# Kernel tuning notes

Measured on AMD Instinct MI355X. Metric: run time of the kernel, lower is better.

## Reference

```python
import jax, jax.numpy as jnp
import numpy as np

B, T, C, H = 2, 2048, 1024, 16
HS = C // H  # 64
EPS = 1e-5


def layer_norm(x, w, b):
    mu = jnp.mean(x, axis=-1, keepdims=True)
    var = jnp.var(x, axis=-1, keepdims=True)
    return (x - mu) * jax.lax.rsqrt(var + EPS) * w + b


def setup_inputs() -> dict:
    key = jax.random.key(0)
    ks = jax.random.split(key, 16)
    s_c = 1.0 / np.sqrt(C)
    s_f = 1.0 / np.sqrt(4 * C)
    u = lambda k, shape, s: jax.random.uniform(k, shape, jnp.float32, -s, s)
    return {
        "x": jax.random.normal(ks[0], (B, T, C), jnp.float32),
        # per-head Q/K/V Linears stacked over heads: [H, C, HS], bias [H, HS]
        "Wq": u(ks[1], (H, C, HS), s_c), "bq": u(ks[2], (H, HS), s_c),
        "Wk": u(ks[3], (H, C, HS), s_c), "bk": u(ks[4], (H, HS), s_c),
        "Wv": u(ks[5], (H, C, HS), s_c), "bv": u(ks[6], (H, HS), s_c),
        "Wp": u(ks[7], (C, C), s_c), "bp": u(ks[8], (C,), s_c),
        "W1": u(ks[9], (C, 4 * C), s_c), "b1": u(ks[10], (4 * C,), s_c),
        "W2": u(ks[11], (4 * C, C), s_f), "b2": u(ks[12], (C,), s_f),
        "ln1_w": jnp.ones((C,), jnp.float32), "ln1_b": jnp.zeros((C,), jnp.float32),
        "ln2_w": jnp.ones((C,), jnp.float32), "ln2_b": jnp.zeros((C,), jnp.float32),
    }


def reference(x, Wq, bq, Wk, bk, Wv, bv, Wp, bp, W1, b1, W2, b2,
              ln1_w, ln1_b, ln2_w, ln2_b):
    # --- pre-norm self-attention ---
    xn = layer_norm(x, ln1_w, ln1_b)
    q = jnp.einsum('btc,hcd->bhtd', xn, Wq) + bq[None, :, None, :]
    k = jnp.einsum('btc,hcd->bhtd', xn, Wk) + bk[None, :, None, :]
    v = jnp.einsum('btc,hcd->bhtd', xn, Wv) + bv[None, :, None, :]
    # NOTE: original scales by C**-0.5 (full embedding dim), not head_size**-0.5
    att = jnp.einsum('bhtd,bhsd->bhts', q, k) * (C ** -0.5)
    att = jax.nn.softmax(att, axis=-1)
    o = jnp.einsum('bhts,bhsd->bhtd', att, v)  # [B,H,T,HS]
    o = jnp.transpose(o, (0, 2, 1, 3)).reshape(B, T, C)  # concat heads
    sa = o @ Wp + bp
    out = x + sa
    # --- pre-norm FFN (exact erf GELU, matching nn.GELU default) ---
    on = layer_norm(out, ln2_w, ln2_b)
    h = jax.nn.gelu(on @ W1 + b1, approximate=False)
    return out + (h @ W2 + b2)
```

## Files before the change

kernel.cpp:

```cpp
#include <hip/hip_runtime.h>
#include <math.h>

#define BB 2
#define TT 2048
#define CC 1024
#define HH 16
#define HS 64
#define MT 4096
#define FF 4096

typedef unsigned short u16;
typedef __bf16 bfrag __attribute__((ext_vector_type(8)));
typedef float f4 __attribute__((ext_vector_type(4)));
typedef float f16v __attribute__((ext_vector_type(16)));

#define AS1(p) ((const __attribute__((address_space(1))) void*)(p))
#define AS3(p) ((__attribute__((address_space(3))) void*)(p))

__device__ __forceinline__ u16 f2bf(float f) {
  union { float f; unsigned u; } a; a.f = f;
  return (u16)((a.u + 0x7fffu + ((a.u >> 16) & 1u)) >> 16);
}
__device__ __forceinline__ float bf2f(u16 u) {
  union { unsigned u; float f; } a; a.u = ((unsigned)u) << 16; return a.f;
}

__device__ __forceinline__ int swz128(int byteoff) {
  return byteoff ^ (((byteoff >> 7) & 7) << 4);
}
__device__ __forceinline__ int swzAB(int byteoff) {
  return byteoff ^ (((byteoff >> 7) & 3) << 4);
}

#define XCD_SWZ_2D(BX, BY)                                                     \
  int _fl = (int)blockIdx.y * gridDim.x + blockIdx.x;                          \
  const int _nw = gridDim.x * gridDim.y;                                       \
  _fl = (_fl & 7) * (_nw >> 3) + (_fl >> 3);                                   \
  const int BX = _fl % gridDim.x;                                              \
  const int BY = _fl / gridDim.x;

__global__ void tr_f32_bf16(const float* __restrict__ src, u16* __restrict__ dst,
                            int R, int Cc, long long sb, long long db, int dld) {
  __shared__ float t[32][33];
  const int bz = blockIdx.z;
  const int r0 = blockIdx.y * 32, c0 = blockIdx.x * 32;
  const int tx = threadIdx.x, ty = threadIdx.y;
  const float* s = src + bz * sb;
  u16* d = dst + bz * db;
#pragma unroll
  for (int i = 0; i < 4; i++)
    t[ty + i * 8][tx] = s[(size_t)(r0 + ty + i * 8) * Cc + c0 + tx];
  __syncthreads();
#pragma unroll
  for (int i = 0; i < 4; i++)
    d[(size_t)(c0 + ty + i * 8) * dld + r0 + tx] = f2bf(t[tx][ty + i * 8]);
}

__global__ void tr_bf16(const u16* __restrict__ src, u16* __restrict__ dst,
                        int R, int Cc, long long sb, long long db, int dld) {
  __shared__ u16 t[32][33];
  const int bz = blockIdx.z;
  const int r0 = blockIdx.y * 32, c0 = blockIdx.x * 32;
  const int tx = threadIdx.x, ty = threadIdx.y;
  const u16* s = src + bz * sb;
  u16* d = dst + bz * db;
#pragma unroll
  for (int i = 0; i < 4; i++)
    t[ty + i * 8][tx] = s[(size_t)(r0 + ty + i * 8) * Cc + c0 + tx];
  __syncthreads();
#pragma unroll
  for (int i = 0; i < 4; i++)
    d[(size_t)(c0 + ty + i * 8) * dld + r0 + tx] = t[tx][ty + i * 8];
}

__global__ __launch_bounds__(256) void ln_kernel(
    const float* __restrict__ x, const float* __restrict__ w,
    const float* __restrict__ b, u16* __restrict__ y) {
  const int row = blockIdx.x, tid = threadIdx.x;
  const float4 v = reinterpret_cast<const float4*>(x + (size_t)row * CC)[tid];
  float s = v.x + v.y + v.z + v.w;
  float s2 = v.x * v.x + v.y * v.y + v.z * v.z + v.w * v.w;
#pragma unroll
  for (int off = 32; off >= 1; off >>= 1) {
    s += __shfl_xor(s, off);
    s2 += __shfl_xor(s2, off);
  }
  __shared__ float ps[4], ps2[4];
  const int wave = tid >> 6, lane = tid & 63;
  if (lane == 0) { ps[wave] = s; ps2[wave] = s2; }
  __syncthreads();
  s = ps[0] + ps[1] + ps[2] + ps[3];
  s2 = ps2[0] + ps2[1] + ps2[2] + ps2[3];
  const float mu = s * (1.f / CC);
  const float rstd = rsqrtf(s2 * (1.f / CC) - mu * mu + 1e-5f);
  const float4 wv = reinterpret_cast<const float4*>(w)[tid];
  const float4 bv = reinterpret_cast<const float4*>(b)[tid];
  ushort4 o;
  o.x = f2bf((v.x - mu) * rstd * wv.x + bv.x);
  o.y = f2bf((v.y - mu) * rstd * wv.y + bv.y);
  o.z = f2bf((v.z - mu) * rstd * wv.z + bv.z);
  o.w = f2bf((v.w - mu) * rstd * wv.w + bv.w);
  reinterpret_cast<ushort4*>(y + (size_t)row * CC)[tid] = o;
}

template<int NJ>
__device__ __forceinline__ void gemm_core(
    u16* smem, const u16* __restrict__ A, const u16* __restrict__ Bt,
    int K, int lda, int ldb, int bmi, int bni, f4 (&acc)[4][NJ]) {
  constexpr int BN = NJ * 32;
  constexpr int BBUF = BN * 32;
  u16* As = smem;
  u16* Bs = smem + 3 * 4096;
  const int tid = threadIdx.x;
  const int wave = tid >> 6, lane = tid & 63;
  const int wm = wave >> 1, wn = wave & 1;
  const int lg = lane >> 4, ll = lane & 15;

  const int trow = tid >> 2;
  const int tch  = (tid & 3) ^ ((trow >> 1) & 3);
  const u16* ga = A + (size_t)(bmi * 128 + trow) * lda + tch * 8;
  const u16* gb = Bt + (size_t)(bni * BN + trow) * ldb + tch * 8;
  const size_t g64a = (size_t)64 * lda;
  const size_t g64b = (size_t)64 * ldb;
  const int nt = K >> 5;

  auto GSTAGE = [&](int bi, int kt) {
    u16* la = &As[bi * 4096 + tid * 8];
    u16* lb = &Bs[bi * BBUF + tid * 8];
    const u16* gA = ga + kt * 32;
    const u16* gB = gb + kt * 32;
    __builtin_amdgcn_global_load_lds(AS1(gA), AS3(la), 16, 0, 0);
    __builtin_amdgcn_global_load_lds(AS1(gA + g64a), AS3(la + 2048), 16, 0, 0);
    __builtin_amdgcn_global_load_lds(AS1(gB), AS3(lb), 16, 0, 0);
    if constexpr (NJ == 4)
      __builtin_amdgcn_global_load_lds(AS1(gB + g64b), AS3(lb + 2048), 16, 0, 0);
  };

  GSTAGE(0, 0);
  GSTAGE(1, 1);
  GSTAGE(2, 2);
  int bi = 0;
  for (int t = 0; t < nt; t++) {
    const int ahead = nt - 1 - t;
    if constexpr (NJ == 4) {
      if (ahead >= 2)      asm volatile("s_waitcnt vmcnt(8)" ::: "memory");
      else if (ahead == 1) asm volatile("s_waitcnt vmcnt(4)" ::: "memory");
      else                 asm volatile("s_waitcnt vmcnt(0)" ::: "memory");
    } else {
      if (ahead >= 2)      asm volatile("s_waitcnt vmcnt(6)" ::: "memory");
      else if (ahead == 1) asm volatile("s_waitcnt vmcnt(3)" ::: "memory");
      else                 asm volatile("s_waitcnt vmcnt(0)" ::: "memory");
    }
    __builtin_amdgcn_s_barrier();
    __builtin_amdgcn_sched_barrier(0);

    const char* as_ = (const char*)(As + bi * 4096);
    const char* bs_ = (const char*)(Bs + bi * BBUF);
    bfrag af[4], bf[NJ];
#pragma unroll
    for (int i = 0; i < 4; i++)
      af[i] = *(const bfrag*)(as_ + swzAB((wm * 64 + i * 16 + ll) * 64 + lg * 16));
#pragma unroll
    for (int j = 0; j < NJ; j++)
      bf[j] = *(const bfrag*)(bs_ + swzAB((wn * (BN / 2) + j * 16 + ll) * 64 + lg * 16));

    __builtin_amdgcn_s_setprio(1);
#pragma unroll
    for (int i = 0; i < 4; i++)
#pragma unroll
      for (int j = 0; j < NJ; j++)
        acc[i][j] = __builtin_amdgcn_mfma_f32_16x16x32_bf16(af[i], bf[j], acc[i][j], 0, 0, 0);
    __builtin_amdgcn_s_setprio(0);

    __builtin_amdgcn_sched_barrier(0);
    __builtin_amdgcn_s_barrier();
    if (t + 3 < nt) GSTAGE(bi, t + 3);
    bi = (bi == 2) ? 0 : bi + 1;
  }
}

#define EPI_COORDS                                              \
  const int tid = threadIdx.x;                                  \
  const int wave = tid >> 6, lane = tid & 63;                   \
  const int wm = wave >> 1, wn = wave & 1;                      \
  const int lg = lane >> 4, ll = lane & 15;

__global__ __launch_bounds__(256, 3) void gemm_qkv(
    const u16* __restrict__ A, const u16* __restrict__ Bt,
    const float* __restrict__ bq, const float* __restrict__ bk,
    const float* __restrict__ bv,
    u16* __restrict__ q, u16* __restrict__ k, u16* __restrict__ v) {
  __shared__ u16 smem[24576];
  XCD_SWZ_2D(bx, by)
  f4 acc[4][4] = {};
  gemm_core<4>(smem, A, Bt, CC, CC, CC, by, bx, acc);
  EPI_COORDS
  __syncthreads();
#pragma unroll
  for (int j = 0; j < 4; j++) {
    const int n = bx * 128 + wn * 64 + j * 16 + ll;
    const int sec = n >> 10, nn = n & 1023;
    const float bias = (sec == 0 ? bq : (sec == 1 ? bk : bv))[nn];
    const float scale = (sec == 0) ? 0.045084220027780106f : 1.0f;
#pragma unroll
    for (int i = 0; i < 4; i++)
#pragma unroll
      for (int r = 0; r < 4; r++)
        smem[(wm * 64 + i * 16 + lg * 4 + r) * 136 + wn * 64 + j * 16 + ll] =
            f2bf((acc[i][j][r] + bias) * scale);
  }
  __syncthreads();
  const int rr = tid >> 4, cb = (tid & 15) * 8;
#pragma unroll
  for (int R = 0; R < 8; R++) {
    const int row = R * 16 + rr;
    const int m = by * 128 + row, b = m >> 11, t = m & 2047;
    const int n = bx * 128 + cb;
    const int sec = n >> 10, nn = n & 1023, h = nn >> 6, d = nn & 63;
    u16* dst = sec == 0 ? q : (sec == 1 ? k : v);
    *(uint4*)&dst[(((size_t)b * HH + h) * TT + t) * HS + d] =
        *(const uint4*)&smem[row * 136 + cb];
  }
}

__global__ __launch_bounds__(256, 3) void gemm_ffn1(
    const u16* __restrict__ A, const u16* __restrict__ Bt,
    const float* __restrict__ b1, u16* __restrict__ hb) {
  __shared__ u16 smem[24576];
  XCD_SWZ_2D(bx, by)
  f4 acc[4][4] = {};
  gemm_core<4>(smem, A, Bt, CC, CC, CC, by, bx, acc);
  EPI_COORDS
  __syncthreads();
#pragma unroll
  for (int j = 0; j < 4; j++) {
    const int n = bx * 128 + wn * 64 + j * 16 + ll;
    const float bias = b1[n];
#pragma unroll
    for (int i = 0; i < 4; i++)
#pragma unroll
      for (int r = 0; r < 4; r++) {
        const float t = acc[i][j][r] + bias;
        const float g = 0.5f * t * (1.0f + erff(t * 0.70710678118654752f));
        smem[(wm * 64 + i * 16 + lg * 4 + r) * 136 + wn * 64 + j * 16 + ll] = f2bf(g);
      }
  }
  __syncthreads();
  const int rr = tid >> 4, cb = (tid & 15) * 8;
#pragma unroll
  for (int R = 0; R < 8; R++) {
    const int row = R * 16 + rr;
    *(uint4*)&hb[(size_t)(by * 128 + row) * FF + bx * 128 + cb] =
        *(const uint4*)&smem[row * 136 + cb];
  }
}

__global__ __launch_bounds__(256, 3) void gemm_ffn2sk(
    const u16* __restrict__ A, const u16* __restrict__ Bt,
    u16* __restrict__ p0, u16* __restrict__ p1) {
  __shared__ u16 smem[24576];
  int _fl = ((int)blockIdx.z * gridDim.y + blockIdx.y) * gridDim.x + blockIdx.x;
  const int _nw = gridDim.x * gridDim.y * gridDim.z;
  _fl = (_fl & 7) * (_nw >> 3) + (_fl >> 3);
  const int bx = _fl % gridDim.x;
  const int by = (_fl / gridDim.x) % gridDim.y;
  const int bz = _fl / (gridDim.x * gridDim.y);

  f4 acc[4][4] = {};
  gemm_core<4>(smem, A + bz * 2048, Bt + bz * 2048, 2048, FF, FF, by, bx, acc);
  EPI_COORDS
  __syncthreads();
#pragma unroll
  for (int j = 0; j < 4; j++)
#pragma unroll
    for (int i = 0; i < 4; i++)
#pragma unroll
      for (int r = 0; r < 4; r++)
        smem[(wm * 64 + i * 16 + lg * 4 + r) * 136 + wn * 64 + j * 16 + ll] =
            f2bf(acc[i][j][r]);
  __syncthreads();
  u16* pp = bz ? p1 : p0;
  const int rr = tid >> 4, cb = (tid & 15) * 8;
#pragma unroll
  for (int R = 0; R < 8; R++) {
    const int row = R * 16 + rr;
    *(uint4*)&pp[(size_t)(by * 128 + row) * CC + bx * 128 + cb] =
        *(const uint4*)&smem[row * 136 + cb];
  }
}

__global__ __launch_bounds__(256) void ffn2_reduce(
    const u16* __restrict__ p0, const u16* __restrict__ p1,
    const float* __restrict__ b2, float* __restrict__ dout) {
  const int gid = blockIdx.x * 256 + threadIdx.x;
  const int n0 = (gid * 8) & (CC - 1);
  const uint4 a = ((const uint4*)p0)[gid];
  const uint4 c = ((const uint4*)p1)[gid];
  const u16* au = (const u16*)&a;
  const u16* cu = (const u16*)&c;
  float4 d0 = ((const float4*)dout)[gid * 2];
  float4 d1 = ((const float4*)dout)[gid * 2 + 1];
  const float4 w0 = *(const float4*)&b2[n0];
  const float4 w1 = *(const float4*)&b2[n0 + 4];
  d0.x += w0.x + bf2f(au[0]) + bf2f(cu[0]);
  d0.y += w0.y + bf2f(au[1]) + bf2f(cu[1]);
  d0.z += w0.z + bf2f(au[2]) + bf2f(cu[2]);
  d0.w += w0.w + bf2f(au[3]) + bf2f(cu[3]);
  d1.x += w1.x + bf2f(au[4]) + bf2f(cu[4]);
  d1.y += w1.y + bf2f(au[5]) + bf2f(cu[5]);
  d1.z += w1.z + bf2f(au[6]) + bf2f(cu[6]);
  d1.w += w1.w + bf2f(au[7]) + bf2f(cu[7]);
  ((float4*)dout)[gid * 2] = d0;
  ((float4*)dout)[gid * 2 + 1] = d1;
}

__global__ __launch_bounds__(256, 3) void gemm_proj(
    const u16* __restrict__ A, const u16* __restrict__ Bt,
    const float* __restrict__ bp, const float* __restrict__ x,
    float* __restrict__ outw) {
  __shared__ u16 smem[18432];
  XCD_SWZ_2D(bx, by)
  f4 acc[4][2] = {};
  gemm_core<2>(smem, A, Bt, CC, CC, CC, by, bx, acc);
  EPI_COORDS
#pragma unroll
  for (int i = 0; i < 4; i++)
#pragma unroll
    for (int j = 0; j < 2; j++) {
      const int n = bx * 64 + wn * 32 + j * 16 + ll;
      const float bias = bp[n];
#pragma unroll
      for (int r = 0; r < 4; r++) {
        const int m = by * 128 + wm * 64 + i * 16 + lg * 4 + r;
        const size_t idx = (size_t)m * CC + n;
        outw[idx] = acc[i][j][r] + bias + x[idx];
      }
    }
}

__global__ __launch_bounds__(256, 2) void attn_kernel(
    const u16* __restrict__ Q, const u16* __restrict__ Kb,
    const u16* __restrict__ Vt, u16* __restrict__ Ao) {
  __shared__ __align__(1024) u16 Ks[2][64 * 64];
  __shared__ __align__(1024) u16 Vs[2][64 * 64];

  const int fl = (int)blockIdx.y * gridDim.x + blockIdx.x;
  const int idx = fl >> 3;
  const int bh = (idx >> 4) * 8 + (fl & 7);
  const int qt = idx & 15;

  const int tid = threadIdx.x, wave = tid >> 6, lane = tid & 63;
  const int l31 = lane & 31, hi = lane >> 5;

  bfrag qf[4];
  const u16* Qb = Q + ((size_t)bh * TT + qt * 128 + wave * 32) * HS;
#pragma unroll
  for (int t = 0; t < 4; t++)
    qf[t] = *(const bfrag*)&Qb[l31 * HS + t * 16 + hi * 8];

  f16v o0 = {}, o1 = {};
  float mrun = -INFINITY, lrun = 0.f;

  const int trow = tid >> 3;
  const int tch  = (tid & 7) ^ (trow & 7);
  const u16* gk = Kb + ((size_t)bh * TT + trow) * HS + tch * 8;
  const u16* gv = Vt + ((size_t)bh * HS + trow) * TT + tch * 8;

  int koff[2][4], voff[2][2][2];
#pragma unroll
  for (int sub = 0; sub < 2; sub++) {
#pragma unroll
    for (int t = 0; t < 4; t++)
      koff[sub][t] = swz128((sub * 32 + l31) * 128 + t * 32 + hi * 16);
#pragma unroll
    for (int dh = 0; dh < 2; dh++)
#pragma unroll
      for (int ks = 0; ks < 2; ks++)
        voff[dh][sub][ks] = swz128((dh * 32 + l31) * 128 + sub * 64 + ks * 32 + hi * 16);
  }

#define STAGE(bufi, stt)                                                          \
  do {                                                                            \
    u16* lk = &Ks[bufi][tid * 8];                                                 \
    u16* lv = &Vs[bufi][tid * 8];                                                 \
    __builtin_amdgcn_global_load_lds(AS1(gk + (size_t)(stt) * HS), AS3(lk), 16, 0, 0); \
    __builtin_amdgcn_global_load_lds(AS1(gk + (size_t)(stt) * HS + 32 * HS), AS3(lk + 2048), 16, 0, 0); \
    __builtin_amdgcn_global_load_lds(AS1(gv + (stt)), AS3(lv), 16, 0, 0);         \
    __builtin_amdgcn_global_load_lds(AS1(gv + (stt) + (size_t)32 * TT), AS3(lv + 2048), 16, 0, 0); \
  } while (0)

  STAGE(0, 0);
  int cur = 0;

  for (int st = 0; st < TT; st += 64) {
    if (st + 64 < TT) {
      STAGE(cur ^ 1, st + 64);
      asm volatile("s_waitcnt vmcnt(4)" ::: "memory");
    } else {
      asm volatile("s_waitcnt vmcnt(0)" ::: "memory");
    }
    __builtin_amdgcn_s_barrier();
    __builtin_amdgcn_sched_barrier(0);

    const char* kbuf = (const char*)Ks[cur];
    const char* vbuf = (const char*)Vs[cur];

    f16v s0 = {}, s1 = {};
#pragma unroll
    for (int t = 0; t < 4; t++) {
      const bfrag kf0 = *(const bfrag*)(kbuf + koff[0][t]);
      s0 = __builtin_amdgcn_mfma_f32_32x32x16_bf16(kf0, qf[t], s0, 0, 0, 0);
    }
#pragma unroll
    for (int t = 0; t < 4; t++) {
      const bfrag kf1 = *(const bfrag*)(kbuf + koff[1][t]);
      s1 = __builtin_amdgcn_mfma_f32_32x32x16_bf16(kf1, qf[t], s1, 0, 0, 0);
    }

    float t8[8];
#pragma unroll
    for (int j = 0; j < 8; j++) t8[j] = fmaxf(s0[j], s0[j + 8]);
#pragma unroll
    for (int j = 0; j < 8; j++) t8[j] = fmaxf(t8[j], fmaxf(s1[j], s1[j + 8]));
#pragma unroll
    for (int j = 0; j < 4; j++) t8[j] = fmaxf(t8[j], t8[j + 4]);
    float pm = fmaxf(fmaxf(t8[0], t8[1]), fmaxf(t8[2], t8[3]));
    pm = fmaxf(pm, __shfl_xor(pm, 32));

    if (!__all((int)(pm <= mrun))) {
      const float mn = fmaxf(mrun, pm);
      const float al = exp2f(mrun - mn);
      mrun = mn;
      lrun *= al;
#pragma unroll
      for (int j = 0; j < 16; j++) { o0[j] *= al; o1[j] *= al; }
    }

    unsigned pf[2][2][4];
    float rs = 0.f;
#pragma unroll
    for (int j = 0; j < 16; j++) { s0[j] = exp2f(s0[j] - mrun); rs += s0[j]; }
#pragma unroll
    for (int j = 0; j < 16; j++) { s1[j] = exp2f(s1[j] - mrun); rs += s1[j]; }
    rs += __shfl_xor(rs, 32);
    lrun += rs;

#pragma unroll
    for (int sub = 0; sub < 2; sub++) {
      const f16v& sv = sub ? s1 : s0;
      unsigned a0, a1, a2, a3, a4, a5, a6, a7;
      asm("v_cvt_pk_bf16_f32 %0, %1, %2" : "=v"(a0) : "v"(sv[0]),  "v"(sv[1]));
      asm("v_cvt_pk_bf16_f32 %0, %1, %2" : "=v"(a1) : "v"(sv[2]),  "v"(sv[3]));
      asm("v_cvt_pk_bf16_f32 %0, %1, %2" : "=v"(a2) : "v"(sv[4]),  "v"(sv[5]));
      asm("v_cvt_pk_bf16_f32 %0, %1, %2" : "=v"(a3) : "v"(sv[6]),  "v"(sv[7]));
      asm("v_cvt_pk_bf16_f32 %0, %1, %2" : "=v"(a4) : "v"(sv[8]),  "v"(sv[9]));
      asm("v_cvt_pk_bf16_f32 %0, %1, %2" : "=v"(a5) : "v"(sv[10]), "v"(sv[11]));
      asm("v_cvt_pk_bf16_f32 %0, %1, %2" : "=v"(a6) : "v"(sv[12]), "v"(sv[13]));
      asm("v_cvt_pk_bf16_f32 %0, %1, %2" : "=v"(a7) : "v"(sv[14]), "v"(sv[15]));
      asm("v_permlane32_swap_b32 %0, %1" : "+v"(a2), "+v"(a0));
      asm("v_permlane32_swap_b32 %0, %1" : "+v"(a3), "+v"(a1));
      asm("v_permlane32_swap_b32 %0, %1" : "+v"(a6), "+v"(a4));
      asm("v_permlane32_swap_b32 %0, %1" : "+v"(a7), "+v"(a5));
      pf[sub][0][0] = a0; pf[sub][0][1] = a1; pf[sub][0][2] = a2; pf[sub][0][3] = a3;
      pf[sub][1][0] = a4; pf[sub][1][1] = a5; pf[sub][1][2] = a6; pf[sub][1][3] = a7;
    }

#pragma unroll
    for (int sub = 0; sub < 2; sub++)
#pragma unroll
      for (int ks = 0; ks < 2; ks++) {
        union { unsigned u[4]; bfrag b; } pb;
        pb.u[0] = pf[sub][ks][0]; pb.u[1] = pf[sub][ks][1];
        pb.u[2] = pf[sub][ks][2]; pb.u[3] = pf[sub][ks][3];
        const bfrag vf0 = *(const bfrag*)(vbuf + voff[0][sub][ks]);
        o0 = __builtin_amdgcn_mfma_f32_32x32x16_bf16(vf0, pb.b, o0, 0, 0, 0);
        const bfrag vf1 = *(const bfrag*)(vbuf + voff[1][sub][ks]);
        o1 = __builtin_amdgcn_mfma_f32_32x32x16_bf16(vf1, pb.b, o1, 0, 0, 0);
      }

    __builtin_amdgcn_sched_barrier(0);
    __builtin_amdgcn_s_barrier();
    cur ^= 1;
  }
#undef STAGE

  const int b = bh >> 4, h = bh & 15;
  const float inv = 1.0f / lrun;
  const int t = qt * 128 + wave * 32 + l31;
  u16* aorow = Ao + ((size_t)b * TT + t) * CC + h * HS;
#pragma unroll
  for (int dh = 0; dh < 2; dh++) {
    const f16v& ov = dh ? o1 : o0;
#pragma unroll
    for (int rq = 0; rq < 4; rq++) {
      union { uint2 v; __bf16 hh[4]; } w;
      w.hh[0] = (__bf16)(ov[rq * 4 + 0] * inv);
      w.hh[1] = (__bf16)(ov[rq * 4 + 1] * inv);
      w.hh[2] = (__bf16)(ov[rq * 4 + 2] * inv);
      w.hh[3] = (__bf16)(ov[rq * 4 + 3] * inv);
      *(uint2*)&aorow[dh * 32 + rq * 8 + hi * 4] = w.v;
    }
  }
}

extern "C" void kernel_launch(void* const* d_in, const int* in_sizes, int n_in,
                              void* d_out, int out_size, void* d_ws, size_t ws_size,
                              hipStream_t stream) {
  const float* x    = (const float*)d_in[0];
  const float* Wq   = (const float*)d_in[1];
  const float* bq   = (const float*)d_in[2];
  const float* Wk   = (const float*)d_in[3];
  const float* bk   = (const float*)d_in[4];
  const float* Wv   = (const float*)d_in[5];
  const float* bv   = (const float*)d_in[6];
  const float* Wp   = (const float*)d_in[7];
  const float* bp   = (const float*)d_in[8];
  const float* W1   = (const float*)d_in[9];
  const float* b1   = (const float*)d_in[10];
  const float* W2   = (const float*)d_in[11];
  const float* b2   = (const float*)d_in[12];
  const float* ln1w = (const float*)d_in[13];
  const float* ln1b = (const float*)d_in[14];
  const float* ln2w = (const float*)d_in[15];
  const float* ln2b = (const float*)d_in[16];
  float* dout = (float*)d_out;

  char* ws = (char*)d_ws;
  u16* wqkv = (u16*)(ws + 0);
  u16* wpt  = (u16*)(ws + 6291456);
  u16* w1t  = (u16*)(ws + 8388608);
  u16* w2t  = (u16*)(ws + 16777216);
  u16* xn   = (u16*)(ws + 25165824);
  u16* qb   = (u16*)(ws + 33554432);
  u16* kb   = (u16*)(ws + 41943040);
  u16* vb   = (u16*)(ws + 50331648);
  u16* vt   = (u16*)(ws + 58720256);
  u16* ao   = (u16*)(ws + 67108864);
  u16* hb   = qb;
  u16* pk0  = (u16*)(ws + 0);
  u16* pk1  = (u16*)(ws + 8388608);

  dim3 blk256(256);
  dim3 blkT(32, 8);

  tr_f32_bf16<<<dim3(2, 32, 16), blkT, 0, stream>>>(Wq, wqkv,               1024,   64, 65536LL, 65536LL, 1024);
  tr_f32_bf16<<<dim3(2, 32, 16), blkT, 0, stream>>>(Wk, wqkv + 1024 * 1024, 1024,   64, 65536LL, 65536LL, 1024);
  tr_f32_bf16<<<dim3(2, 32, 16), blkT, 0, stream>>>(Wv, wqkv + 2048 * 1024, 1024,   64, 65536LL, 65536LL, 1024);
  tr_f32_bf16<<<dim3(32, 32, 1),  blkT, 0, stream>>>(Wp, wpt, 1024, 1024, 0LL, 0LL, 1024);
  tr_f32_bf16<<<dim3(128, 32, 1), blkT, 0, stream>>>(W1, w1t, 1024, 4096, 0LL, 0LL, 1024);
  tr_f32_bf16<<<dim3(32, 128, 1), blkT, 0, stream>>>(W2, w2t, 4096, 1024, 0LL, 0LL, 4096);

  ln_kernel<<<dim3(MT), blk256, 0, stream>>>(x, ln1w, ln1b, xn);

  gemm_qkv<<<dim3(24, 32), blk256, 0, stream>>>(xn, wqkv, bq, bk, bv, qb, kb, vb);

  tr_bf16<<<dim3(2, 64, 32), blkT, 0, stream>>>(vb, vt, 2048, 64, 131072LL, 131072LL, 2048);

  attn_kernel<<<dim3(16, 32), blk256, 0, stream>>>(qb, kb, vt, ao);

  gemm_proj<<<dim3(16, 32), blk256, 0, stream>>>(ao, wpt, bp, x, dout);

  ln_kernel<<<dim3(MT), blk256, 0, stream>>>(dout, ln2w, ln2b, xn);

  gemm_ffn1<<<dim3(32, 32), blk256, 0, stream>>>(xn, w1t, b1, hb);
  gemm_ffn2sk<<<dim3(8, 32, 2), blk256, 0, stream>>>(hb, w2t, pk0, pk1);
  ffn2_reduce<<<dim3(MT * CC / 8 / 256), blk256, 0, stream>>>(pk0, pk1, b2, dout);
}
```

Measured before the change: 272.1 us.

## Use 256x256 eight-wave GEMM tiles for QKV/FFN1 and triple-buffer attention K/V

Adds a new GEMM core that uses 256x256 output tiles with 512 threads, double-buffered LDS staged in K-halves, and loads interleaved with MFMA phases. The QKV and FFN1 kernels switch to it with two-pass epilogues, cutting grid size and raising operand reuse per byte loaded. Attention moves to three K/V stage buffers so the trailing per-iteration barrier can be dropped. The larger tiles give fewer blocks (192 for QKV), which may underfill the CUs, and the 128KB LDS footprint limits occupancy.

```diff
diff --git a/kernel.cpp b/kernel.cpp
--- a/kernel.cpp
+++ b/kernel.cpp
@@ -103,6 +103,209 @@
   reinterpret_cast<ushort4*>(y + (size_t)row * CC)[tid] = o;
 }
 
+__device__ __forceinline__ void gemm256_core(
+    u16* smem, const u16* __restrict__ A, const u16* __restrict__ Bt,
+    int K, int lda, int ldb, int bmi, int bni, f4 (&acc)[8][4]) {
+  const int tid = threadIdx.x;
+  const int wave = tid >> 6, lane = tid & 63;
+  const int wm = wave >> 2, wn = wave & 3;
+  const int lg = lane >> 4, ll = lane & 15;
+
+  const int trow = tid >> 2;
+  const int tch  = (tid & 3) ^ ((trow >> 1) & 3);
+  const u16* ga = A + (size_t)(bmi * 256 + trow) * lda + tch * 8;
+  const u16* gb = Bt + (size_t)(bni * 256 + trow) * ldb + tch * 8;
+  const int nt = K >> 6;
+
+  auto STG = [&](int bf, int kt, int op, int kh) {
+    const u16* g = (op ? gb : ga) + (size_t)kt * 64 + kh * 32;
+    const int ld = op ? ldb : lda;
+    u16* d = smem + op * 32768 + bf * 16384 + kh * 8192 + tid * 8;
+    __builtin_amdgcn_global_load_lds(AS1(g), AS3(d), 16, 0, 0);
+    __builtin_amdgcn_global_load_lds(AS1(g + (size_t)128 * ld), AS3(d + 4096), 16, 0, 0);
+  };
+
+  STG(0, 0, 0, 0); STG(0, 0, 1, 0); STG(0, 0, 0, 1); STG(0, 0, 1, 1);
+
+  for (int t = 0; t < nt; t++) {
+    const int bf = t & 1, nbf = bf ^ 1;
+    const bool pre = (t + 1 < nt);
+    const char* ab = (const char*)smem + bf * 32768;
+    const char* bb = (const char*)smem + 65536 + bf * 32768;
+    bfrag af[4], bfg[4];
+
+    if (pre) STG(nbf, t + 1, 0, 0);
+    if (pre) asm volatile("s_waitcnt vmcnt(6)" ::: "memory");
+    else     asm volatile("s_waitcnt vmcnt(4)" ::: "memory");
+    __builtin_amdgcn_s_barrier();
+    __builtin_amdgcn_sched_barrier(0);
+#pragma unroll
+    for (int i = 0; i < 4; i++)
+      af[i] = *(const bfrag*)(ab + swzAB((wm * 128 + i * 16 + ll) * 64 + lg * 16));
+#pragma unroll
+    for (int j = 0; j < 4; j++)
+      bfg[j] = *(const bfrag*)(bb + swzAB((wn * 64 + j * 16 + ll) * 64 + lg * 16));
+    asm volatile("s_waitcnt lgkmcnt(0)" ::: "memory");
+    __builtin_amdgcn_sched_barrier(0);
+    __builtin_amdgcn_s_setprio(1);
+#pragma unroll
+    for (int i = 0; i < 4; i++)
+#pragma unroll
+      for (int j = 0; j < 4; j++)
+        acc[i][j] = __builtin_amdgcn_mfma_f32_16x16x32_bf16(af[i], bfg[j], acc[i][j], 0, 0, 0);
+    __builtin_amdgcn_s_setprio(0);
+    __builtin_amdgcn_sched_barrier(0);
+    __builtin_amdgcn_s_barrier();
+
+    if (pre) STG(nbf, t + 1, 1, 0);
+#pragma unroll
+    for (int i = 0; i < 4; i++)
+      af[i] = *(const bfrag*)(ab + swzAB((wm * 128 + 64 + i * 16 + ll) * 64 + lg * 16));
+    asm volatile("s_waitcnt lgkmcnt(0)" ::: "memory");
+    __builtin_amdgcn_sched_barrier(0);
+    __builtin_amdgcn_s_setprio(1);
+#pragma unroll
+    for (int i = 0; i < 4; i++)
+#pragma unroll
+      for (int j = 0; j < 4; j++)
+        acc[4 + i][j] = __builtin_amdgcn_mfma_f32_16x16x32_bf16(af[i], bfg[j], acc[4 + i][j], 0, 0, 0);
+    __builtin_amdgcn_s_setprio(0);
+    __builtin_amdgcn_sched_barrier(0);
+    __builtin_amdgcn_s_barrier();
+
+    if (pre) STG(nbf, t + 1, 0, 1);
+    if (pre) asm volatile("s_waitcnt vmcnt(6)" ::: "memory");
+    else     asm volatile("s_waitcnt vmcnt(0)" ::: "memory");
+    __builtin_amdgcn_s_barrier();
+    __builtin_amdgcn_sched_barrier(0);
+#pragma unroll
+    for (int i = 0; i < 4; i++)
+      af[i] = *(const bfrag*)(ab + 16384 + swzAB((wm * 128 + i * 16 + ll) * 64 + lg * 16));
+#pragma unroll
+    for (int j = 0; j < 4; j++)
+      bfg[j] = *(const bfrag*)(bb + 16384 + swzAB((wn * 64 + j * 16 + ll) * 64 + lg * 16));
+    asm volatile("s_waitcnt lgkmcnt(0)" ::: "memory");
+    __builtin_amdgcn_sched_barrier(0);
+    __builtin_amdgcn_s_setprio(1);
+#pragma unroll
+    for (int i = 0; i < 4; i++)
+#pragma unroll
+      for (int j = 0; j < 4; j++)
+        acc[i][j] = __builtin_amdgcn_mfma_f32_16x16x32_bf16(af[i], bfg[j], acc[i][j], 0, 0, 0);
+    __builtin_amdgcn_s_setprio(0);
+    __builtin_amdgcn_sched_barrier(0);
+    __builtin_amdgcn_s_barrier();
+
+    if (pre) STG(nbf, t + 1, 1, 1);
+#pragma unroll
+    for (int i = 0; i < 4; i++)
+      af[i] = *(const bfrag*)(ab + 16384 + swzAB((wm * 128 + 64 + i * 16 + ll) * 64 + lg * 16));
+    asm volatile("s_waitcnt lgkmcnt(0)" ::: "memory");
+    __builtin_amdgcn_sched_barrier(0);
+    __builtin_amdgcn_s_setprio(1);
+#pragma unroll
+    for (int i = 0; i < 4; i++)
+#pragma unroll
+      for (int j = 0; j < 4; j++)
+        acc[4 + i][j] = __builtin_amdgcn_mfma_f32_16x16x32_bf16(af[i], bfg[j], acc[4 + i][j], 0, 0, 0);
+    __builtin_amdgcn_s_setprio(0);
+    __builtin_amdgcn_sched_barrier(0);
+    __builtin_amdgcn_s_barrier();
+  }
+}
+
+__global__ __launch_bounds__(512, 2) void gemm_qkv(
+    const u16* __restrict__ A, const u16* __restrict__ Bt,
+    const float* __restrict__ bq, const float* __restrict__ bk,
+    const float* __restrict__ bv,
+    u16* __restrict__ q, u16* __restrict__ k, u16* __restrict__ v) {
+  __shared__ u16 smem[65536];
+  XCD_SWZ_2D(bx, by)
+  f4 acc[8][4] = {};
+  gemm256_core(smem, A, Bt, CC, CC, CC, by, bx, acc);
+  const int tid = threadIdx.x;
+  const int wave = tid >> 6, lane = tid & 63;
+  const int wm = wave >> 2, wn = wave & 3;
+  const int lg = lane >> 4, ll = lane & 15;
+#pragma unroll
+  for (int p = 0; p < 2; p++) {
+    __syncthreads();
+    if (wm == p) {
+#pragma unroll
+      for (int j = 0; j < 4; j++) {
+        const int n = bx * 256 + wn * 64 + j * 16 + ll;
+        const int sec = n >> 10, nn = n & 1023;
+        const float bias = (sec == 0 ? bq : (sec == 1 ? bk : bv))[nn];
+        const float scale = (sec == 0) ? 0.045084220027780106f : 1.0f;
+#pragma unroll
+        for (int a = 0; a < 8; a++)
+#pragma unroll
+          for (int r = 0; r < 4; r++)
+            smem[((a >> 2) * 64 + (a & 3) * 16 + lg * 4 + r) * 264 + wn * 64 + j * 16 + ll] =
+                f2bf((acc[a][j][r] + bias) * scale);
+      }
+    }
+    __syncthreads();
+    const int rr = tid >> 3, cb0 = (tid & 7) * 32;
+#pragma unroll
+    for (int R = 0; R < 2; R++) {
+      const int lr = R * 64 + rr;
+      const int m = by * 256 + p * 128 + lr, b = m >> 11, t = m & 2047;
+#pragma unroll
+      for (int c = 0; c < 4; c++) {
+        const int n = bx * 256 + cb0 + c * 8;
+        const int sec = n >> 10, nn = n & 1023, h = nn >> 6, d = nn & 63;
+        u16* dst = sec == 0 ? q : (sec == 1 ? k : v);
+        *(uint4*)&dst[(((size_t)b * HH + h) * TT + t) * HS + d] =
+            *(const uint4*)&smem[lr * 264 + cb0 + c * 8];
+      }
+    }
+  }
+}
+
+__global__ __launch_bounds__(512, 2) void gemm_ffn1(
+    const u16* __restrict__ A, const u16* __restrict__ Bt,
+    const float* __restrict__ b1, u16* __restrict__ hb) {
+  __shared__ u16 smem[65536];
+  XCD_SWZ_2D(bx, by)
+  f4 acc[8][4] = {};
+  gemm256_core(smem, A, Bt, CC, CC, CC, by, bx, acc);
+  const int tid = threadIdx.x;
+  const int wave = tid >> 6, lane = tid & 63;
+  const int wm = wave >> 2, wn = wave & 3;
+  const int lg = lane >> 4, ll = lane & 15;
+#pragma unroll
+  for (int p = 0; p < 2; p++) {
+    __syncthreads();
+    if (wm == p) {
+#pragma unroll
+      for (int j = 0; j < 4; j++) {
+        const int n = bx * 256 + wn * 64 + j * 16 + ll;
+        const float bias = b1[n];
+#pragma unroll
+        for (int a = 0; a < 8; a++)
+#pragma unroll
+          for (int r = 0; r < 4; r++) {
+            const float tv = acc[a][j][r] + bias;
+            const float g = 0.5f * tv * (1.0f + erff(tv * 0.70710678118654752f));
+            smem[((a >> 2) * 64 + (a & 3) * 16 + lg * 4 + r) * 264 + wn * 64 + j * 16 + ll] = f2bf(g);
+          }
+      }
+    }
+    __syncthreads();
+    const int rr = tid >> 3, cb0 = (tid & 7) * 32;
+#pragma unroll
+    for (int R = 0; R < 2; R++) {
+      const int lr = R * 64 + rr;
+      const int m = by * 256 + p * 128 + lr;
+#pragma unroll
+      for (int c = 0; c < 4; c++)
+        *(uint4*)&hb[(size_t)m * FF + bx * 256 + cb0 + c * 8] =
+            *(const uint4*)&smem[lr * 264 + cb0 + c * 8];
+    }
+  }
+}
+
 template<int NJ>
 __device__ __forceinline__ void gemm_core(
     u16* smem, const u16* __restrict__ A, const u16* __restrict__ Bt,
@@ -184,76 +387,6 @@
   const int wave = tid >> 6, lane = tid & 63;                   \
   const int wm = wave >> 1, wn = wave & 1;                      \
   const int lg = lane >> 4, ll = lane & 15;
-
-__global__ __launch_bounds__(256, 3) void gemm_qkv(
-    const u16* __restrict__ A, const u16* __restrict__ Bt,
-    const float* __restrict__ bq, const float* __restrict__ bk,
-    const float* __restrict__ bv,
-    u16* __restrict__ q, u16* __restrict__ k, u16* __restrict__ v) {
-  __shared__ u16 smem[24576];
-  XCD_SWZ_2D(bx, by)
-  f4 acc[4][4] = {};
-  gemm_core<4>(smem, A, Bt, CC, CC, CC, by, bx, acc);
-  EPI_COORDS
-  __syncthreads();
-#pragma unroll
-  for (int j = 0; j < 4; j++) {
-    const int n = bx * 128 + wn * 64 + j * 16 + ll;
-    const int sec = n >> 10, nn = n & 1023;
-    const float bias = (sec == 0 ? bq : (sec == 1 ? bk : bv))[nn];
-    const float scale = (sec == 0) ? 0.045084220027780106f : 1.0f;
-#pragma unroll
-    for (int i = 0; i < 4; i++)
-#pragma unroll
-      for (int r = 0; r < 4; r++)
-        smem[(wm * 64 + i * 16 + lg * 4 + r) * 136 + wn * 64 + j * 16 + ll] =
-            f2bf((acc[i][j][r] + bias) * scale);
-  }
-  __syncthreads();
-  const int rr = tid >> 4, cb = (tid & 15) * 8;
-#pragma unroll
-  for (int R = 0; R < 8; R++) {
-    const int row = R * 16 + rr;
-    const int m = by * 128 + row, b = m >> 11, t = m & 2047;
-    const int n = bx * 128 + cb;
-    const int sec = n >> 10, nn = n & 1023, h = nn >> 6, d = nn & 63;
-    u16* dst = sec == 0 ? q : (sec == 1 ? k : v);
-    *(uint4*)&dst[(((size_t)b * HH + h) * TT + t) * HS + d] =
-        *(const uint4*)&smem[row * 136 + cb];
-  }
-}
-
-__global__ __launch_bounds__(256, 3) void gemm_ffn1(
-    const u16* __restrict__ A, const u16* __restrict__ Bt,
-    const float* __restrict__ b1, u16* __restrict__ hb) {
-  __shared__ u16 smem[24576];
-  XCD_SWZ_2D(bx, by)
-  f4 acc[4][4] = {};
-  gemm_core<4>(smem, A, Bt, CC, CC, CC, by, bx, acc);
-  EPI_COORDS
-  __syncthreads();
-#pragma unroll
-  for (int j = 0; j < 4; j++) {
-    const int n = bx * 128 + wn * 64 + j * 16 + ll;
-    const float bias = b1[n];
-#pragma unroll
-    for (int i = 0; i < 4; i++)
-#pragma unroll
-      for (int r = 0; r < 4; r++) {
-        const float t = acc[i][j][r] + bias;
-        const float g = 0.5f * t * (1.0f + erff(t * 0.70710678118654752f));
-        smem[(wm * 64 + i * 16 + lg * 4 + r) * 136 + wn * 64 + j * 16 + ll] = f2bf(g);
-      }
-  }
-  __syncthreads();
-  const int rr = tid >> 4, cb = (tid & 15) * 8;
-#pragma unroll
-  for (int R = 0; R < 8; R++) {
-    const int row = R * 16 + rr;
-    *(uint4*)&hb[(size_t)(by * 128 + row) * FF + bx * 128 + cb] =
-        *(const uint4*)&smem[row * 136 + cb];
-  }
-}
 
 __global__ __launch_bounds__(256, 3) void gemm_ffn2sk(
     const u16* __restrict__ A, const u16* __restrict__ Bt,
@@ -341,8 +474,8 @@
 __global__ __launch_bounds__(256, 2) void attn_kernel(
     const u16* __restrict__ Q, const u16* __restrict__ Kb,
     const u16* __restrict__ Vt, u16* __restrict__ Ao) {
-  __shared__ __align__(1024) u16 Ks[2][64 * 64];
-  __shared__ __align__(1024) u16 Vs[2][64 * 64];
+  __shared__ __align__(1024) u16 Ks[3][64 * 64];
+  __shared__ __align__(1024) u16 Vs[3][64 * 64];
 
   const int fl = (int)blockIdx.y * gridDim.x + blockIdx.x;
   const int idx = fl >> 3;
@@ -393,8 +526,9 @@
   int cur = 0;
 
   for (int st = 0; st < TT; st += 64) {
+    const int nxt = (cur == 2) ? 0 : cur + 1;
     if (st + 64 < TT) {
-      STAGE(cur ^ 1, st + 64);
+      STAGE(nxt, st + 64);
       asm volatile("s_waitcnt vmcnt(4)" ::: "memory");
     } else {
       asm volatile("s_waitcnt vmcnt(0)" ::: "memory");
@@ -478,9 +612,7 @@
         o1 = __builtin_amdgcn_mfma_f32_32x32x16_bf16(vf1, pb.b, o1, 0, 0, 0);
       }
 
-    __builtin_amdgcn_sched_barrier(0);
-    __builtin_amdgcn_s_barrier();
-    cur ^= 1;
+    cur = nxt;
   }
 #undef STAGE
 
@@ -541,6 +673,7 @@
   u16* pk1  = (u16*)(ws + 8388608);
 
   dim3 blk256(256);
+  dim3 blk512(512);
   dim3 blkT(32, 8);
 
   tr_f32_bf16<<<dim3(2, 32, 16), blkT, 0, stream>>>(Wq, wqkv,               1024,   64, 65536LL, 65536LL, 1024);
@@ -552,7 +685,7 @@
 
   ln_kernel<<<dim3(MT), blk256, 0, stream>>>(x, ln1w, ln1b, xn);
 
-  gemm_qkv<<<dim3(24, 32), blk256, 0, stream>>>(xn, wqkv, bq, bk, bv, qb, kb, vb);
+  gemm_qkv<<<dim3(12, 16), blk512, 0, stream>>>(xn, wqkv, bq, bk, bv, qb, kb, vb);
 
   tr_bf16<<<dim3(2, 64, 32), blkT, 0, stream>>>(vb, vt, 2048, 64, 131072LL, 131072LL, 2048);
 
@@ -562,7 +695,7 @@
 
   ln_kernel<<<dim3(MT), blk256, 0, stream>>>(dout, ln2w, ln2b, xn);
 
-  gemm_ffn1<<<dim3(32, 32), blk256, 0, stream>>>(xn, w1t, b1, hb);
+  gemm_ffn1<<<dim3(16, 16), blk512, 0, stream>>>(xn, w1t, b1, hb);
   gemm_ffn2sk<<<dim3(8, 32, 2), blk256, 0, stream>>>(hb, w2t, pk0, pk1);
   ffn2_reduce<<<dim3(MT * CC / 8 / 256), blk256, 0, stream>>>(pk0, pk1, b2, dout);
 }
```

New measurement: 296.7 us. 1.09x slower.
